# Kernel tuning notes

Measured on AMD Instinct MI355X. Metric: run time of the kernel, lower is better.

The kernel has to match this reference:

```python
import jax, jax.numpy as jnp
import numpy as np

C0, C1, C2 = 2000, 10000, 50000  # class cutoffs
D = 1024                          # input_size (hidden dim)
OUT_HEAD = C0 + 2                 # head output: shortlist + 2 cluster logits


def setup_inputs() -> dict:
    key = jax.random.key(0)
    ks = jax.random.split(key, 7)
    s = lambda fan_in: 1.0 / np.sqrt(fan_in)
    x = jax.random.normal(ks[0], (4096, D), dtype=jnp.float32)
    Wh = jax.random.normal(ks[1], (OUT_HEAD, D), dtype=jnp.float32) * s(D)
    bh = jnp.zeros((OUT_HEAD,), dtype=jnp.float32)
    # tail 0: D -> D//4**0 -> (C1-C0)
    W0a = jax.random.normal(ks[2], (D, D), dtype=jnp.float32) * s(D)
    W0b = jax.random.normal(ks[3], (C1 - C0, D), dtype=jnp.float32) * s(D)
    # tail 1: D -> D//4**1 -> (C2-C1)
    W1a = jax.random.normal(ks[4], (D // 4, D), dtype=jnp.float32) * s(D)
    W1b = jax.random.normal(ks[5], (C2 - C1, D // 4), dtype=jnp.float32) * s(D // 4)
    return {"x": x, "Wh": Wh, "bh": bh, "W0a": W0a, "W0b": W0b, "W1a": W1a, "W1b": W1b}


def reference(x, Wh, bh, W0a, W0b, W1a, W1b):
    # head: [B, OUT_HEAD]; log-softmax over shortlist + cluster logits
    lsm_head = jax.nn.log_softmax(x @ Wh.T + bh, axis=-1)
    # tail clusters: capacity-reduction linear, projection, log-softmax within cluster
    lsm_t0 = jax.nn.log_softmax((x @ W0a.T) @ W0b.T, axis=-1)  # [B, C1-C0]
    lsm_t1 = jax.nn.log_softmax((x @ W1a.T) @ W1b.T, axis=-1)  # [B, C2-C1]
    # flat log-probs: cluster log-prob broadcast-added to within-cluster log-probs
    prob = jnp.concatenate([
        lsm_head[:, :C0],
        lsm_head[:, C0:C0 + 1] + lsm_t0,
        lsm_head[:, C0 + 1:C0 + 2] + lsm_t1,
    ], axis=1)  # [B, C2]
    return prob
```

## Files before the change

### kernel.cpp

```cpp
#include <hip/hip_runtime.h>
#include <hip/hip_bf16.h>
#include <math.h>

#define CC0 2000
#define CC1 10000
#define CC2 50000
#define DH  1024
#define BATCH 4096
#define OUT_HEAD (CC0 + 2)

#define N0_P 8192
#define N1_P 40192
#define NH_P 2048

typedef __attribute__((ext_vector_type(4))) float  f32x4;
typedef __attribute__((ext_vector_type(8))) __bf16 bf16x8;
typedef __attribute__((ext_vector_type(8))) short  s16x8;

__device__ __forceinline__ void gload_lds16(const void* g, void* l) {
    __builtin_amdgcn_global_load_lds(
        (const __attribute__((address_space(1))) void*)g,
        (__attribute__((address_space(3))) void*)l, 16, 0, 0);
}

__device__ __forceinline__ float bf2f(unsigned short u) {
    return __builtin_bit_cast(float, (unsigned)u << 16);
}

__global__ __launch_bounds__(256) void convert_all_kernel(
    const float4* __restrict__ s0, ushort4* __restrict__ d0, int n0s, int n0d,
    const float4* __restrict__ s1, ushort4* __restrict__ d1, int n1s, int n1d,
    const float4* __restrict__ s2, ushort4* __restrict__ d2, int n2s, int n2d,
    const float4* __restrict__ s3, ushort4* __restrict__ d3, int n3s, int n3d,
    const float4* __restrict__ s4, ushort4* __restrict__ d4, int n4s, int n4d,
    const float4* __restrict__ s5, ushort4* __restrict__ d5, int n5s, int n5d)
{
    const float4* src; ushort4* dst; int ns, nd;
    switch (blockIdx.y) {
        case 0: src = s0; dst = d0; ns = n0s; nd = n0d; break;
        case 1: src = s1; dst = d1; ns = n1s; nd = n1d; break;
        case 2: src = s2; dst = d2; ns = n2s; nd = n2d; break;
        case 3: src = s3; dst = d3; ns = n3s; nd = n3d; break;
        case 4: src = s4; dst = d4; ns = n4s; nd = n4d; break;
        default: src = s5; dst = d5; ns = n5s; nd = n5d; break;
    }
    int i = blockIdx.x * blockDim.x + threadIdx.x;
    const int stride = gridDim.x * blockDim.x;
    for (; i < nd; i += stride) {
        ushort4 o = {0, 0, 0, 0};
        if (i < ns) {
            float4 v = src[i];
            o.x = __builtin_bit_cast(unsigned short, (__bf16)v.x);
            o.y = __builtin_bit_cast(unsigned short, (__bf16)v.y);
            o.z = __builtin_bit_cast(unsigned short, (__bf16)v.z);
            o.w = __builtin_bit_cast(unsigned short, (__bf16)v.w);
        }
        dst[i] = o;
    }
}

__global__ __launch_bounds__(256) void gemm128x3_kernel(
    const ushort* __restrict__ x_bf,
    const ushort* __restrict__ W0a_bf, ushort* __restrict__ h0,
    const ushort* __restrict__ W1a_bf, ushort* __restrict__ h1,
    const ushort* __restrict__ Wh_bf,  float*  __restrict__ headL)
{
    __shared__ ushort As[128 * 64];
    __shared__ ushort Bs[128 * 64];

    const int gb = blockIdx.x;
    const ushort* B; void* C;
    int N, ldC, wmode, nbx, lin;
    const int K = DH;
    if (gb < 256)      { B = W0a_bf; C = h0;    N = DH;       ldC = DH;       wmode = 1; nbx = 8;  lin = gb; }
    else if (gb < 320) { B = W1a_bf; C = h1;    N = 256;      ldC = 256;      wmode = 1; nbx = 2;  lin = gb - 256; }
    else               { B = Wh_bf;  C = headL; N = OUT_HEAD; ldC = OUT_HEAD; wmode = 2; nbx = 16; lin = gb - 320; }

    const int nwg = nbx * 32;
    const int q = nwg >> 3;
    int bid = (lin & 7) * q + (lin >> 3);
    const int bx = bid % nbx;
    const int by = bid / nbx;

    const int t = threadIdx.x;
    const int lane = t & 63;
    const int w = t >> 6;
    const int wr = w >> 1, wc = w & 1;
    const int lr = lane & 15;
    const int lg = lane >> 4;
    const int bm = by * 128;
    const int bn = bx * 128;
    const int lrow = lane >> 3;
    const int lcol = (lane & 7) * 8;

    f32x4 acc[4][4] = {};

    for (int k0 = 0; k0 < K; k0 += 64) {
        #pragma unroll
        for (int i = 0; i < 4; ++i) {
            const int seg = w * 4 + i;
            const int row = seg * 8 + lrow;
            gload_lds16(x_bf + (size_t)(bm + row) * K + k0 + lcol, &As[seg * 512]);
            gload_lds16(B + (size_t)(bn + row) * K + k0 + lcol, &Bs[seg * 512]);
        }
        __syncthreads();
        #pragma unroll
        for (int ks = 0; ks < 2; ++ks) {
            s16x8 af[4], bfr[4];
            #pragma unroll
            for (int m = 0; m < 4; ++m)
                af[m] = *(const s16x8*)&As[(wr * 64 + m * 16 + lr) * 64 + ks * 32 + lg * 8];
            #pragma unroll
            for (int n = 0; n < 4; ++n)
                bfr[n] = *(const s16x8*)&Bs[(wc * 64 + n * 16 + lr) * 64 + ks * 32 + lg * 8];
            #pragma unroll
            for (int m = 0; m < 4; ++m)
                #pragma unroll
                for (int n = 0; n < 4; ++n)
                    acc[m][n] = __builtin_amdgcn_mfma_f32_16x16x32_bf16(
                        __builtin_bit_cast(bf16x8, af[m]),
                        __builtin_bit_cast(bf16x8, bfr[n]), acc[m][n], 0, 0, 0);
        }
        __syncthreads();
    }

    #pragma unroll
    for (int m = 0; m < 4; ++m)
        #pragma unroll
        for (int r = 0; r < 4; ++r) {
            const int row = bm + wr * 64 + m * 16 + lg * 4 + r;
            #pragma unroll
            for (int n = 0; n < 4; ++n) {
                const int col = bn + wc * 64 + n * 16 + lr;
                float v = acc[m][n][r];
                if (col < N) {
                    if (wmode == 1)
                        ((ushort*)C)[(size_t)row * ldC + col] =
                            __builtin_bit_cast(unsigned short, (__bf16)v);
                    else
                        ((float*)C)[(size_t)row * ldC + col] = v;
                }
            }
        }
}

__global__ __launch_bounds__(512, 1) void tails256_kernel(
    const ushort* __restrict__ h0, const ushort* __restrict__ W0b,
    ushort* __restrict__ L0,
    const ushort* __restrict__ h1, const ushort* __restrict__ W1b,
    ushort* __restrict__ L1)
{
    __shared__ ushort lds[2][2][256 * 64];

    const int gb = blockIdx.x;
    const ushort *A, *B; ushort* C;
    int K, N, nbx, ldC, lin;
    if (gb < 512) { A = h0; B = W0b; C = L0; K = DH;  N = CC1 - CC0; nbx = N0_P / 256; ldC = N0_P; lin = gb; }
    else          { A = h1; B = W1b; C = L1; K = 256; N = CC2 - CC1; nbx = N1_P / 256; ldC = N1_P; lin = gb - 512; }

    const int nwg = nbx * 16;
    const int q8 = nwg >> 3;
    int bid = (lin & 7) * q8 + (lin >> 3);
    const int by = bid % 16;
    const int bx = bid / 16;
    const int bm = by * 256, bn = bx * 256;

    const int t = threadIdx.x;
    const int lane = t & 63;
    const int w = t >> 6;
    const int wr = w >> 2;
    const int wc = w & 3;
    const int lr = lane & 15;
    const int lg = lane >> 4;
    const int xr = (lr & 7) << 4;
    const int c0 = w * 64 + lane;

    f32x4 acc[8][4] = {};
    const int nkt = K / 64;

    auto stage_chunk = [&](int ktile, int buf, int p) {
        const int k0 = ktile * 64;
        const int mat = (p == 1 || p == 2) ? 1 : 0;
        const int j = (p == 3) ? 1 : (p == 2 ? 1 : 0);
        const ushort* gbase = mat ? B : A;
        const int brow = mat ? bn : bm;
        #pragma unroll
        for (int i = 0; i < 2; ++i) {
            const int v = i * 512 + c0;
            const int vrow = v >> 3;
            int ar;
            if (mat == 0) ar = ((vrow >> 6) << 7) + (j << 6) + (vrow & 63);
            else          ar = ((vrow >> 5) << 6) + (j << 5) + (vrow & 31);
            const int cc = (v & 7) ^ (ar & 7);
            const int v0 = (i * 512 + w * 64) >> 3;
            int ar0;
            if (mat == 0) ar0 = ((v0 >> 6) << 7) + (j << 6) + (v0 & 63);
            else          ar0 = ((v0 >> 5) << 6) + (j << 5) + (v0 & 31);
            gload_lds16(gbase + (size_t)(brow + ar) * K + k0 + cc * 8,
                        (char*)&lds[buf][mat][0] + ar0 * 128);
        }
    };

    #pragma unroll
    for (int p = 0; p < 4; ++p) stage_chunk(0, 0, p);
    asm volatile("s_waitcnt vmcnt(0)" ::: "memory");
    __builtin_amdgcn_s_barrier();
    asm volatile("" ::: "memory");

    for (int tk = 0; tk < nkt; ++tk) {
        const int cur = tk & 1;
        const char* baseA = (const char*)&lds[cur][0][0];
        const char* baseB = (const char*)&lds[cur][1][0];
        const bool more = (tk + 1 < nkt);

        s16x8 bq[4][2];
        s16x8 af[4][2];

        #pragma unroll
        for (int p = 0; p < 4; ++p) {
            const int mh = p >> 1, nh = p & 1;
            if (more) {
                stage_chunk(tk + 1, cur ^ 1, p);
                asm volatile("s_waitcnt vmcnt(6)" ::: "memory");
            } else {
                if (p == 0)      asm volatile("s_waitcnt vmcnt(4)" ::: "memory");
                else if (p == 1) asm volatile("s_waitcnt vmcnt(2)" ::: "memory");
                else if (p == 2) asm volatile("s_waitcnt vmcnt(0)" ::: "memory");
            }
            __builtin_amdgcn_s_barrier();
            asm volatile("" ::: "memory");

            if (p == 0 || p == 2) {
                #pragma unroll
                for (int m_ = 0; m_ < 4; ++m_) {
                    const int row = wr * 128 + (mh * 4 + m_) * 16 + lr;
                    #pragma unroll
                    for (int ks = 0; ks < 2; ++ks)
                        af[m_][ks] = *(const s16x8*)(baseA + (row * 128 + ((ks * 64 + lg * 16) ^ xr)));
                }
            }
            if (p == 0 || p == 1) {
                #pragma unroll
                for (int n_ = 0; n_ < 2; ++n_) {
                    const int row = wc * 64 + (p * 2 + n_) * 16 + lr;
                    #pragma unroll
                    for (int ks = 0; ks < 2; ++ks)
                        bq[p * 2 + n_][ks] = *(const s16x8*)(baseB + (row * 128 + ((ks * 64 + lg * 16) ^ xr)));
                }
            }
            __builtin_amdgcn_s_setprio(1);
            #pragma unroll
            for (int m_ = 0; m_ < 4; ++m_)
                #pragma unroll
                for (int n_ = 0; n_ < 2; ++n_)
                    #pragma unroll
                    for (int ks = 0; ks < 2; ++ks)
                        acc[mh * 4 + m_][nh * 2 + n_] = __builtin_amdgcn_mfma_f32_16x16x32_bf16(
                            __builtin_bit_cast(bf16x8, af[m_][ks]),
                            __builtin_bit_cast(bf16x8, bq[nh * 2 + n_][ks]),
                            acc[mh * 4 + m_][nh * 2 + n_], 0, 0, 0);
            __builtin_amdgcn_s_setprio(0);
        }
    }

    #pragma unroll
    for (int m = 0; m < 8; ++m) {
        #pragma unroll
        for (int r = 0; r < 4; ++r) {
            const int row = bm + wr * 128 + m * 16 + lg * 4 + r;
            #pragma unroll
            for (int n = 0; n < 4; ++n) {
                const int col = bn + wc * 64 + n * 16 + lr;
                if (col < N)
                    C[(size_t)row * ldC + col] =
                        __builtin_bit_cast(unsigned short, (__bf16)acc[m][n][r]);
            }
        }
    }
}

__global__ __launch_bounds__(512) void finalize_rows_kernel(
    const float* __restrict__ HL, const float* __restrict__ bh,
    const ushort* __restrict__ L0, const ushort* __restrict__ L1,
    float* __restrict__ out)
{
    const int row = blockIdx.x;
    const int t = threadIdx.x;
    const float* L = HL + (size_t)row * OUT_HEAD;
    const ushort* r0 = L0 + (size_t)row * N0_P;
    const ushort* r1 = L1 + (size_t)row * N1_P;
    float* o = out + (size_t)row * CC2;
    __shared__ float redh[8], red0[8], red1[8], bc[3];

    float hv[4];
    s16x8 v0[2], v1[10];
    float hs = 0.f, p0 = 0.f, p1 = 0.f;
    #pragma unroll
    for (int k = 0; k < 4; ++k) {
        const int i = t + k * 512;
        float v = 0.f;
        if (i < OUT_HEAD) { v = L[i] + bh[i]; hs += __expf(v); }
        hv[k] = v;
    }
    #pragma unroll
    for (int k = 0; k < 2; ++k) {
        const int c = t + k * 512;
        if (c < 1000) {
            v0[k] = *(const s16x8*)(r0 + c * 8);
            #pragma unroll
            for (int j = 0; j < 8; ++j) p0 += __expf(bf2f((unsigned short)v0[k][j]));
        }
    }
    #pragma unroll
    for (int k = 0; k < 10; ++k) {
        const int c = t + k * 512;
        if (c < 5000) {
            v1[k] = *(const s16x8*)(r1 + c * 8);
            #pragma unroll
            for (int j = 0; j < 8; ++j) p1 += __expf(bf2f((unsigned short)v1[k][j]));
        }
    }

    #pragma unroll
    for (int s = 1; s < 64; s <<= 1) {
        hs += __shfl_xor(hs, s, 64);
        p0 += __shfl_xor(p0, s, 64);
        p1 += __shfl_xor(p1, s, 64);
    }
    if ((t & 63) == 0) { redh[t >> 6] = hs; red0[t >> 6] = p0; red1[t >> 6] = p1; }
    __syncthreads();
    if (t == 0) {
        float sh = 0.f, s0 = 0.f, s1 = 0.f;
        #pragma unroll
        for (int i = 0; i < 8; ++i) { sh += redh[i]; s0 += red0[i]; s1 += red1[i]; }
        const float lse = logf(sh);
        bc[2] = lse;
        bc[0] = (L[CC0 + 0] + bh[CC0 + 0] - lse) - logf(s0);
        bc[1] = (L[CC0 + 1] + bh[CC0 + 1] - lse) - logf(s1);
    }
    __syncthreads();
    const float a0 = bc[0], a1 = bc[1], lse = bc[2];

    #pragma unroll
    for (int k = 0; k < 4; ++k) {
        const int i = t + k * 512;
        if (i < CC0) o[i] = hv[k] - lse;
    }
    #pragma unroll
    for (int k = 0; k < 2; ++k) {
        const int c = t + k * 512;
        if (c < 1000) {
            float* dst = o + CC0 + c * 8;
            float4 o0, o1;
            o0.x = bf2f((unsigned short)v0[k][0]) + a0;
            o0.y = bf2f((unsigned short)v0[k][1]) + a0;
            o0.z = bf2f((unsigned short)v0[k][2]) + a0;
            o0.w = bf2f((unsigned short)v0[k][3]) + a0;
            o1.x = bf2f((unsigned short)v0[k][4]) + a0;
            o1.y = bf2f((unsigned short)v0[k][5]) + a0;
            o1.z = bf2f((unsigned short)v0[k][6]) + a0;
            o1.w = bf2f((unsigned short)v0[k][7]) + a0;
            *(float4*)dst = o0;
            *(float4*)(dst + 4) = o1;
        }
    }
    #pragma unroll
    for (int k = 0; k < 10; ++k) {
        const int c = t + k * 512;
        if (c < 5000) {
            float* dst = o + CC1 + c * 8;
            float4 o0, o1;
            o0.x = bf2f((unsigned short)v1[k][0]) + a1;
            o0.y = bf2f((unsigned short)v1[k][1]) + a1;
            o0.z = bf2f((unsigned short)v1[k][2]) + a1;
            o0.w = bf2f((unsigned short)v1[k][3]) + a1;
            o1.x = bf2f((unsigned short)v1[k][4]) + a1;
            o1.y = bf2f((unsigned short)v1[k][5]) + a1;
            o1.z = bf2f((unsigned short)v1[k][6]) + a1;
            o1.w = bf2f((unsigned short)v1[k][7]) + a1;
            *(float4*)dst = o0;
            *(float4*)(dst + 4) = o1;
        }
    }
}

extern "C" void kernel_launch(void* const* d_in, const int* in_sizes, int n_in,
                              void* d_out, int out_size, void* d_ws, size_t ws_size,
                              hipStream_t stream) {
    const float* x   = (const float*)d_in[0];
    const float* Wh  = (const float*)d_in[1];
    const float* bh  = (const float*)d_in[2];
    const float* W0a = (const float*)d_in[3];
    const float* W0b = (const float*)d_in[4];
    const float* W1a = (const float*)d_in[5];
    const float* W1b = (const float*)d_in[6];
    float* out = (float*)d_out;
    char*  ws  = (char*)d_ws;

    size_t off = 0;
    auto alloc = [&](size_t bytes) { size_t o = off; off += (bytes + 255) & ~(size_t)255; return o; };
    ushort* x_bf   = (ushort*)(ws + alloc((size_t)BATCH * DH * 2));
    ushort* Wh_bf  = (ushort*)(ws + alloc((size_t)NH_P * DH * 2));
    ushort* W0a_bf = (ushort*)(ws + alloc((size_t)DH * DH * 2));
    ushort* W0b_bf = (ushort*)(ws + alloc((size_t)N0_P * DH * 2));
    ushort* W1a_bf = (ushort*)(ws + alloc((size_t)256 * DH * 2));
    ushort* W1b_bf = (ushort*)(ws + alloc((size_t)N1_P * 256 * 2));
    ushort* h0_bf  = (ushort*)(ws + alloc((size_t)BATCH * DH * 2));
    ushort* h1_bf  = (ushort*)(ws + alloc((size_t)BATCH * 256 * 2));
    float*  headL  = (float*)(ws + alloc((size_t)BATCH * OUT_HEAD * 4));
    ushort* L0     = (ushort*)(ws + alloc((size_t)BATCH * N0_P * 2));
    ushort* L1     = (ushort*)(ws + alloc((size_t)BATCH * N1_P * 2));

    convert_all_kernel<<<dim3(1280, 6), 256, 0, stream>>>(
        (const float4*)x,   (ushort4*)x_bf,   BATCH * DH / 4,        BATCH * DH / 4,
        (const float4*)Wh,  (ushort4*)Wh_bf,  OUT_HEAD * DH / 4,     NH_P * DH / 4,
        (const float4*)W0a, (ushort4*)W0a_bf, DH * DH / 4,           DH * DH / 4,
        (const float4*)W0b, (ushort4*)W0b_bf, (CC1 - CC0) * DH / 4,  N0_P * DH / 4,
        (const float4*)W1a, (ushort4*)W1a_bf, 256 * DH / 4,          256 * DH / 4,
        (const float4*)W1b, (ushort4*)W1b_bf, (CC2 - CC1) * 256 / 4, N1_P * 256 / 4);

    gemm128x3_kernel<<<832, 256, 0, stream>>>(
        x_bf, W0a_bf, h0_bf, W1a_bf, h1_bf, Wh_bf, headL);

    tails256_kernel<<<512 + (N1_P / 256) * 16, 512, 0, stream>>>(
        h0_bf, W0b_bf, L0, h1_bf, W1b_bf, L1);

    finalize_rows_kernel<<<BATCH, 512, 0, stream>>>(headL, bh, L0, L1, out);
}
```

Before: 586.3 us.

## Overlap W0b/W1b bf16 conversion with first-stage GEMM blocks

Splits the fp32-to-bf16 conversion so that only the operands of the first GEMM stage (x, Wh, W0a, W1a) are converted up front. The large W0b and W1b conversions move into extra blocks appended to the first GEMM launch, so they run alongside the GEMM tiles. This is meant to hide the conversion's memory traffic behind GEMM compute and shorten the critical path, at the cost of competing with the GEMM for bandwidth and CU slots.

```diff
diff --git a/kernel.cpp b/kernel.cpp
--- a/kernel.cpp
+++ b/kernel.cpp
@@ -27,26 +27,10 @@
     return __builtin_bit_cast(float, (unsigned)u << 16);
 }
 
-__global__ __launch_bounds__(256) void convert_all_kernel(
-    const float4* __restrict__ s0, ushort4* __restrict__ d0, int n0s, int n0d,
-    const float4* __restrict__ s1, ushort4* __restrict__ d1, int n1s, int n1d,
-    const float4* __restrict__ s2, ushort4* __restrict__ d2, int n2s, int n2d,
-    const float4* __restrict__ s3, ushort4* __restrict__ d3, int n3s, int n3d,
-    const float4* __restrict__ s4, ushort4* __restrict__ d4, int n4s, int n4d,
-    const float4* __restrict__ s5, ushort4* __restrict__ d5, int n5s, int n5d)
-{
-    const float4* src; ushort4* dst; int ns, nd;
-    switch (blockIdx.y) {
-        case 0: src = s0; dst = d0; ns = n0s; nd = n0d; break;
-        case 1: src = s1; dst = d1; ns = n1s; nd = n1d; break;
-        case 2: src = s2; dst = d2; ns = n2s; nd = n2d; break;
-        case 3: src = s3; dst = d3; ns = n3s; nd = n3d; break;
-        case 4: src = s4; dst = d4; ns = n4s; nd = n4d; break;
-        default: src = s5; dst = d5; ns = n5s; nd = n5d; break;
-    }
-    int i = blockIdx.x * blockDim.x + threadIdx.x;
-    const int stride = gridDim.x * blockDim.x;
-    for (; i < nd; i += stride) {
+__device__ __forceinline__ void cvt_range(const float4* __restrict__ src,
+                                          ushort4* __restrict__ dst,
+                                          int ns, int nd, int start, int stride) {
+    for (int i = start; i < nd; i += stride) {
         ushort4 o = {0, 0, 0, 0};
         if (i < ns) {
             float4 v = src[i];
@@ -59,16 +43,44 @@
     }
 }
 
-__global__ __launch_bounds__(256) void gemm128x3_kernel(
+__global__ __launch_bounds__(256) void convert_small_kernel(
+    const float4* __restrict__ x,   ushort4* __restrict__ x_bf,
+    const float4* __restrict__ Wh,  ushort4* __restrict__ Wh_bf,
+    const float4* __restrict__ W0a, ushort4* __restrict__ W0a_bf,
+    const float4* __restrict__ W1a, ushort4* __restrict__ W1a_bf)
+{
+    const int start = blockIdx.x * blockDim.x + threadIdx.x;
+    const int stride = gridDim.x * blockDim.x;
+    switch (blockIdx.y) {
+        case 0: cvt_range(x,   x_bf,   BATCH * DH / 4,    BATCH * DH / 4, start, stride); break;
+        case 1: cvt_range(Wh,  Wh_bf,  OUT_HEAD * DH / 4, NH_P * DH / 4,  start, stride); break;
+        case 2: cvt_range(W0a, W0a_bf, DH * DH / 4,       DH * DH / 4,    start, stride); break;
+        default: cvt_range(W1a, W1a_bf, 256 * DH / 4,     256 * DH / 4,   start, stride); break;
+    }
+}
+
+__global__ __launch_bounds__(256) void gemm128x3_conv_kernel(
     const ushort* __restrict__ x_bf,
     const ushort* __restrict__ W0a_bf, ushort* __restrict__ h0,
     const ushort* __restrict__ W1a_bf, ushort* __restrict__ h1,
-    const ushort* __restrict__ Wh_bf,  float*  __restrict__ headL)
+    const ushort* __restrict__ Wh_bf,  float*  __restrict__ headL,
+    const float4* __restrict__ W0b,  ushort4* __restrict__ W0b_bf,
+    const float4* __restrict__ W1b,  ushort4* __restrict__ W1b_bf)
 {
     __shared__ ushort As[128 * 64];
     __shared__ ushort Bs[128 * 64];
 
     const int gb = blockIdx.x;
+    if (gb >= 832) {
+        if (gb < 1344)
+            cvt_range(W0b, W0b_bf, (CC1 - CC0) * DH / 4, N0_P * DH / 4,
+                      (gb - 832) * 256 + threadIdx.x, 512 * 256);
+        else
+            cvt_range(W1b, W1b_bf, (CC2 - CC1) * 256 / 4, N1_P * 256 / 4,
+                      (gb - 1344) * 256 + threadIdx.x, 512 * 256);
+        return;
+    }
+
     const ushort* B; void* C;
     int N, ldC, wmode, nbx, lin;
     const int K = DH;
@@ -411,16 +423,16 @@
     ushort* L0     = (ushort*)(ws + alloc((size_t)BATCH * N0_P * 2));
     ushort* L1     = (ushort*)(ws + alloc((size_t)BATCH * N1_P * 2));
 
-    convert_all_kernel<<<dim3(1280, 6), 256, 0, stream>>>(
-        (const float4*)x,   (ushort4*)x_bf,   BATCH * DH / 4,        BATCH * DH / 4,
-        (const float4*)Wh,  (ushort4*)Wh_bf,  OUT_HEAD * DH / 4,     NH_P * DH / 4,
-        (const float4*)W0a, (ushort4*)W0a_bf, DH * DH / 4,           DH * DH / 4,
-        (const float4*)W0b, (ushort4*)W0b_bf, (CC1 - CC0) * DH / 4,  N0_P * DH / 4,
-        (const float4*)W1a, (ushort4*)W1a_bf, 256 * DH / 4,          256 * DH / 4,
-        (const float4*)W1b, (ushort4*)W1b_bf, (CC2 - CC1) * 256 / 4, N1_P * 256 / 4);
-
-    gemm128x3_kernel<<<832, 256, 0, stream>>>(
-        x_bf, W0a_bf, h0_bf, W1a_bf, h1_bf, Wh_bf, headL);
+    convert_small_kernel<<<dim3(768, 4), 256, 0, stream>>>(
+        (const float4*)x,   (ushort4*)x_bf,
+        (const float4*)Wh,  (ushort4*)Wh_bf,
+        (const float4*)W0a, (ushort4*)W0a_bf,
+        (const float4*)W1a, (ushort4*)W1a_bf);
+
+    gemm128x3_conv_kernel<<<1856, 256, 0, stream>>>(
+        x_bf, W0a_bf, h0_bf, W1a_bf, h1_bf, Wh_bf, headL,
+        (const float4*)W0b, (ushort4*)W0b_bf,
+        (const float4*)W1b, (ushort4*)W1b_bf);
 
     tails256_kernel<<<512 + (N1_P / 256) * 16, 512, 0, stream>>>(
         h0_bf, W0b_bf, L0, h1_bf, W1b_bf, L1);
```

Result: no change. 591.2 us (median of 2 runs) (+0.8%).
